# Optimization experiments

Measured on AMD Instinct MI355X. Metric: run time of the kernel, lower is better.

Reference implementation:

```python
import jax, jax.numpy as jnp
import numpy as np

B, T, EMB, HID, NCLS = 256, 512, 128, 256, 32000


def _forward(X, C_table, U_i, V_i, b_i, U_f, V_f, b_f, U_c, V_c, b_c, U_o, V_o, b_o,
             U_i1, V_i1, b_i1, U_f1, V_f1, b_f1, U_c1, V_c1, b_c1, U_o1, V_o1, b_o1,
             W_w, b_out):
    E = C_table[X]  # [B, T, EMB]
    # Layer 0: in the source, h_t0 and c_t0 are NEVER reassigned inside the loop,
    # so they remain zeros for every timestep. Hence h_t0 @ V_* == 0 and
    # f_t * c_t0 == 0, and layer 0 is time-independent -> vectorize over T.
    i0 = jax.nn.sigmoid(jnp.einsum('bte,eh->bth', E, U_i) + b_i)
    g0 = jnp.tanh(jnp.einsum('bte,eh->bth', E, U_c) + b_c)
    o0 = jax.nn.sigmoid(jnp.einsum('bte,eh->bth', E, U_o) + b_o)
    c0 = i0 * g0               # f_t * c_t0 term is exactly zero
    h0 = o0 * jnp.tanh(c0)     # [B, T, HID]

    # Layer 1: true recurrence over its own (h_t1, c_t1) state, fed by layer-0 h.
    # Computed for faithfulness; the source's output ignores it (results holds h_t).
    def step(carry, x):
        h1, c1 = carry
        i1 = jax.nn.sigmoid(x @ U_i1 + h1 @ V_i1 + b_i1)
        g1 = jnp.tanh(x @ U_c1 + h1 @ V_c1 + b_c1)
        f1 = jax.nn.sigmoid(x @ U_f1 + h1 @ V_f1 + b_f1)
        o1 = jax.nn.sigmoid(x @ U_o1 + h1 @ V_o1 + b_o1)
        c1n = f1 * c1 + i1 * g1
        h1n = o1 * jnp.tanh(c1n)
        return (h1n, c1n), None

    zeros = jnp.zeros((h0.shape[0], HID), dtype=h0.dtype)
    _carry, _ = jax.lax.scan(step, (zeros, zeros), jnp.swapaxes(h0, 0, 1))

    # outputs = results[-1] = layer-0 hidden at the last timestep
    logits = h0[:, -1, :] @ W_w.T + b_out  # [B, NCLS]
    return logits


def setup_inputs() -> dict:
    key = jax.random.key(0)
    ks = jax.random.split(key, 32)

    def p(k, *shape):
        return (jax.random.normal(k, shape, dtype=jnp.float32) * 0.02)

    inp = {
        'X': jax.random.randint(ks[0], (B, T), 0, NCLS, dtype=jnp.int32),
        'C_table': p(ks[1], NCLS, EMB),
        'U_i': p(ks[2], EMB, HID), 'V_i': p(ks[3], HID, HID), 'b_i': p(ks[4], HID),
        'U_f': p(ks[5], EMB, HID), 'V_f': p(ks[6], HID, HID), 'b_f': p(ks[7], HID),
        'U_c': p(ks[8], EMB, HID), 'V_c': p(ks[9], HID, HID), 'b_c': p(ks[10], HID),
        'U_o': p(ks[11], EMB, HID), 'V_o': p(ks[12], HID, HID), 'b_o': p(ks[13], HID),
        'U_i1': p(ks[14], HID, HID), 'V_i1': p(ks[15], HID, HID), 'b_i1': p(ks[16], HID),
        'U_f1': p(ks[17], HID, HID), 'V_f1': p(ks[18], HID, HID), 'b_f1': p(ks[19], HID),
        'U_c1': p(ks[20], HID, HID), 'V_c1': p(ks[21], HID, HID), 'b_c1': p(ks[22], HID),
        'U_o1': p(ks[23], HID, HID), 'V_o1': p(ks[24], HID, HID), 'b_o1': p(ks[25], HID),
        'W_w': p(ks[26], NCLS, HID),
        'b_out': jnp.ones((NCLS,), dtype=jnp.float32),
    }
    return inp


def reference(X, C_table, U_i, V_i, b_i, U_f, V_f, b_f, U_c, V_c, b_c, U_o, V_o, b_o,
              U_i1, V_i1, b_i1, U_f1, V_f1, b_f1, U_c1, V_c1, b_c1, U_o1, V_o1, b_o1,
              W_w, b_out):
    return _forward(X, C_table, U_i, V_i, b_i, U_f, V_f, b_f, U_c, V_c, b_c,
                    U_o, V_o, b_o, U_i1, V_i1, b_i1, U_f1, V_f1, b_f1,
                    U_c1, V_c1, b_c1, U_o1, V_o1, b_o1, W_w, b_out)
```

## Files before the change

kernel.cpp:

```cpp
#include <hip/hip_runtime.h>

#define B_SZ   256
#define T_SZ   512
#define EMB    128
#define HID    256
#define NCLS   32000

typedef __attribute__((ext_vector_type(8))) short short8;
typedef __attribute__((ext_vector_type(4))) float f32x4;

__device__ inline unsigned short bf16rne(float f) {
    union { float f; unsigned int u; } v; v.f = f;
    unsigned int u = v.u;
    u += 0x7FFFu + ((u >> 16) & 1u);
    return (unsigned short)(u >> 16);
}

__device__ inline unsigned pkhi(float lo, float hi) {
    union { float f; unsigned u; } a, b;
    a.f = lo; b.f = hi;
    return ((b.u + 0x8000u) & 0xFFFF0000u) | ((a.u + 0x8000u) >> 16);
}

__global__ __launch_bounds__(256)
void lstm_h_last(const int* __restrict__ X, const float* __restrict__ C_table,
                 const float* __restrict__ U_i, const float* __restrict__ b_i,
                 const float* __restrict__ U_c, const float* __restrict__ b_c,
                 const float* __restrict__ U_o, const float* __restrict__ b_o,
                 unsigned short* __restrict__ hws) {
    __shared__ float e[EMB];
    const int m = blockIdx.x;
    const int k = threadIdx.x;

    const int token = X[(size_t)m * T_SZ + (T_SZ - 1)];
    if (k < EMB) e[k] = C_table[(size_t)token * EMB + k];
    __syncthreads();

    float ai = 0.f, ac = 0.f, ao = 0.f;
    #pragma unroll
    for (int c = 0; c < 4; ++c) {
        float ui[32], uc[32], uo[32];
        #pragma unroll
        for (int j = 0; j < 32; ++j) {
            const int ee = c * 32 + j;
            ui[j] = U_i[ee * HID + k];
            uc[j] = U_c[ee * HID + k];
            uo[j] = U_o[ee * HID + k];
        }
        #pragma unroll
        for (int j = 0; j < 32; ++j)
            asm volatile("" : "+v"(ui[j]), "+v"(uc[j]), "+v"(uo[j]));
        #pragma unroll
        for (int j = 0; j < 32; ++j) {
            const float ev = e[c * 32 + j];
            ai += ev * ui[j]; ac += ev * uc[j]; ao += ev * uo[j];
        }
    }

    const float i0 = 1.f / (1.f + expf(-(ai + b_i[k])));
    const float g0 = tanhf(ac + b_c[k]);
    const float o0 = 1.f / (1.f + expf(-(ao + b_o[k])));
    hws[(size_t)m * HID + k] = bf16rne(o0 * tanhf(i0 * g0));
}

#define BN2 64
#define BK  32

__global__ __launch_bounds__(512, 4)
void logits_gemm(const unsigned short* __restrict__ hws,
                 const float* __restrict__ Ww,
                 const float* __restrict__ b_out,
                 float* __restrict__ out) {
    __shared__ float          Wb[3][BN2 * BK];
    __shared__ unsigned short Hb[3][B_SZ * BK];

    const int t    = threadIdx.x;
    const int wid  = t >> 6;
    const int lane = t & 63;
    const int l15  = lane & 15;
    const int lq   = lane >> 4;

    const int n0 = blockIdx.x * BN2;
    const int m0 = wid * 32;

    auto stageW = [&](int ks, float* wb) {
        const unsigned gu = (lane & 7) ^ (lane >> 3);
        const float* src = Ww + (size_t)(n0 + (wid << 3) + (lane >> 3)) * HID
                              + ks * BK + gu * 4;
        __builtin_amdgcn_global_load_lds(
            (const __attribute__((address_space(1))) unsigned int*)src,
            (__attribute__((address_space(3))) unsigned int*)(wb + (wid << 3) * BK),
            16, 0, 0);
    };
    auto stageH = [&](int ks, unsigned short* hb) {
        #pragma unroll
        for (int ii = 0; ii < 2; ++ii) {
            const int i = (wid << 1) + ii;
            const unsigned gu = (lane & 3) ^ ((lane >> 2) & 3);
            const unsigned short* src = hws + (size_t)((i << 4) + (lane >> 2)) * HID
                                            + ks * BK + gu * 8;
            __builtin_amdgcn_global_load_lds(
                (const __attribute__((address_space(1))) unsigned int*)src,
                (__attribute__((address_space(3))) unsigned int*)(hb + (i << 4) * BK),
                16, 0, 0);
        }
    };

    f32x4 acc[2][4] = {};

    auto computeK = [&](const float* wb, const unsigned short* hb) {
        short8 bh[2];
        #pragma unroll
        for (int mf = 0; mf < 2; ++mf) {
            const int r = m0 + (mf << 4) + l15;
            bh[mf] = *reinterpret_cast<const short8*>(
                hb + r * BK + ((lq ^ (r & 3)) << 3));
        }
        #pragma unroll
        for (int nt = 0; nt < 4; ++nt) {
            const int r  = (nt << 4) + l15;
            const int sw = r & 7;
            const float* rp = wb + r * BK;
            f32x4 w0 = *reinterpret_cast<const f32x4*>(rp + ((((lq << 1)    ) ^ sw) << 2));
            f32x4 w1 = *reinterpret_cast<const f32x4*>(rp + ((((lq << 1) | 1) ^ sw) << 2));
            union { short8 s; unsigned u[4]; } p;
            p.u[0] = pkhi(w0[0], w0[1]);
            p.u[1] = pkhi(w0[2], w0[3]);
            p.u[2] = pkhi(w1[0], w1[1]);
            p.u[3] = pkhi(w1[2], w1[3]);
            #pragma unroll
            for (int mf = 0; mf < 2; ++mf)
                acc[mf][nt] = __builtin_amdgcn_mfma_f32_16x16x32_bf16(
                    p.s, bh[mf], acc[mf][nt], 0, 0, 0);
        }
    };

    stageW(0, Wb[0]); stageH(0, Hb[0]);
    stageW(1, Wb[1]); stageH(1, Hb[1]);

#define KITER(ks, N) do {                                          \
    asm volatile("s_waitcnt vmcnt(" #N ")" ::: "memory");          \
    __builtin_amdgcn_s_barrier();                                  \
    __builtin_amdgcn_sched_barrier(0);                             \
    if ((ks) + 2 < 8) {                                            \
        stageW((ks) + 2, Wb[((ks) + 2) % 3]);                      \
        stageH((ks) + 2, Hb[((ks) + 2) % 3]);                      \
    }                                                              \
    computeK(Wb[(ks) % 3], Hb[(ks) % 3]);                          \
} while (0)

    KITER(0, 3); KITER(1, 3); KITER(2, 3); KITER(3, 3);
    KITER(4, 3); KITER(5, 3); KITER(6, 3); KITER(7, 0);
#undef KITER

    #pragma unroll
    for (int nt = 0; nt < 4; ++nt) {
        const int nc = n0 + (nt << 4) + (lq << 2);
        f32x4 bv = *reinterpret_cast<const f32x4*>(b_out + nc);
        #pragma unroll
        for (int mf = 0; mf < 2; ++mf) {
            f32x4 o = acc[mf][nt] + bv;
            *reinterpret_cast<f32x4*>(
                out + (size_t)(m0 + (mf << 4) + l15) * NCLS + nc) = o;
        }
    }
}

extern "C" void kernel_launch(void* const* d_in, const int* in_sizes, int n_in,
                              void* d_out, int out_size, void* d_ws, size_t ws_size,
                              hipStream_t stream) {
    const int*   X       = (const int*)  d_in[0];
    const float* C_table = (const float*)d_in[1];
    const float* U_i     = (const float*)d_in[2];
    const float* b_i     = (const float*)d_in[4];
    const float* U_c     = (const float*)d_in[8];
    const float* b_c     = (const float*)d_in[10];
    const float* U_o     = (const float*)d_in[11];
    const float* b_o     = (const float*)d_in[13];
    const float* W_w     = (const float*)d_in[26];
    const float* b_out   = (const float*)d_in[27];
    float* out = (float*)d_out;

    unsigned short* hws = (unsigned short*)d_ws;

    lstm_h_last<<<B_SZ, 256, 0, stream>>>(X, C_table, U_i, b_i, U_c, b_c,
                                          U_o, b_o, hws);
    logits_gemm<<<NCLS / BN2, 512, 0, stream>>>(hws, W_w, b_out, out);
}
```

Baseline: 30.39 us.

## Stage full H in LDS in MFMA fragment layout, keep W in registers

The first kernel now writes h in a pre-swizzled MFMA-fragment order, so the GEMM can copy all of H (128KB bf16) into LDS with contiguous loads. Each wave loads its 16 W rows over the full K directly into registers and converts them to bf16 once. It then loops over all 256 M rows, which removes the 3-stage K pipeline and the per-iteration barriers. Each block covers 128 columns instead of 64. The cost is 128KB of LDS per block, which limits occupancy, and a large register footprint.

```diff
diff --git a/kernel.cpp b/kernel.cpp
--- a/kernel.cpp
+++ b/kernel.cpp
@@ -21,6 +21,7 @@
     a.f = lo; b.f = hi;
     return ((b.u + 0x8000u) & 0xFFFF0000u) | ((a.u + 0x8000u) >> 16);
 }
+
 
 __global__ __launch_bounds__(256)
 void lstm_h_last(const int* __restrict__ X, const float* __restrict__ C_table,
@@ -60,19 +61,19 @@
     const float i0 = 1.f / (1.f + expf(-(ai + b_i[k])));
     const float g0 = tanhf(ac + b_c[k]);
     const float o0 = 1.f / (1.f + expf(-(ao + b_o[k])));
-    hws[(size_t)m * HID + k] = bf16rne(o0 * tanhf(i0 * g0));
+    const unsigned short hv = bf16rne(o0 * tanhf(i0 * g0));
+
+    const int frag_id = (m >> 4) * 8 + (k >> 5);
+    const int lane_in = ((k >> 3) & 3) * 16 + (m & 15);
+    hws[frag_id * 512 + lane_in * 8 + (k & 7)] = hv;
 }
 
-#define BN2 64
-#define BK  32
-
-__global__ __launch_bounds__(512, 4)
+__global__ __launch_bounds__(512, 2)
 void logits_gemm(const unsigned short* __restrict__ hws,
                  const float* __restrict__ Ww,
                  const float* __restrict__ b_out,
                  float* __restrict__ out) {
-    __shared__ float          Wb[3][BN2 * BK];
-    __shared__ unsigned short Hb[3][B_SZ * BK];
+    __shared__ unsigned short Hs[B_SZ * HID];
 
     const int t    = threadIdx.x;
     const int wid  = t >> 6;
@@ -80,89 +81,62 @@
     const int l15  = lane & 15;
     const int lq   = lane >> 4;
 
-    const int n0 = blockIdx.x * BN2;
-    const int m0 = wid * 32;
+    const int nbase = blockIdx.x * 128 + wid * 16;
 
-    auto stageW = [&](int ks, float* wb) {
-        const unsigned gu = (lane & 7) ^ (lane >> 3);
-        const float* src = Ww + (size_t)(n0 + (wid << 3) + (lane >> 3)) * HID
-                              + ks * BK + gu * 4;
-        __builtin_amdgcn_global_load_lds(
-            (const __attribute__((address_space(1))) unsigned int*)src,
-            (__attribute__((address_space(3))) unsigned int*)(wb + (wid << 3) * BK),
-            16, 0, 0);
-    };
-    auto stageH = [&](int ks, unsigned short* hb) {
-        #pragma unroll
-        for (int ii = 0; ii < 2; ++ii) {
-            const int i = (wid << 1) + ii;
-            const unsigned gu = (lane & 3) ^ ((lane >> 2) & 3);
-            const unsigned short* src = hws + (size_t)((i << 4) + (lane >> 2)) * HID
-                                            + ks * BK + gu * 8;
-            __builtin_amdgcn_global_load_lds(
-                (const __attribute__((address_space(1))) unsigned int*)src,
-                (__attribute__((address_space(3))) unsigned int*)(hb + (i << 4) * BK),
-                16, 0, 0);
-        }
-    };
-
-    f32x4 acc[2][4] = {};
-
-    auto computeK = [&](const float* wb, const unsigned short* hb) {
-        short8 bh[2];
-        #pragma unroll
-        for (int mf = 0; mf < 2; ++mf) {
-            const int r = m0 + (mf << 4) + l15;
-            bh[mf] = *reinterpret_cast<const short8*>(
-                hb + r * BK + ((lq ^ (r & 3)) << 3));
-        }
-        #pragma unroll
-        for (int nt = 0; nt < 4; ++nt) {
-            const int r  = (nt << 4) + l15;
-            const int sw = r & 7;
-            const float* rp = wb + r * BK;
-            f32x4 w0 = *reinterpret_cast<const f32x4*>(rp + ((((lq << 1)    ) ^ sw) << 2));
-            f32x4 w1 = *reinterpret_cast<const f32x4*>(rp + ((((lq << 1) | 1) ^ sw) << 2));
-            union { short8 s; unsigned u[4]; } p;
-            p.u[0] = pkhi(w0[0], w0[1]);
-            p.u[1] = pkhi(w0[2], w0[3]);
-            p.u[2] = pkhi(w1[0], w1[1]);
-            p.u[3] = pkhi(w1[2], w1[3]);
-            #pragma unroll
-            for (int mf = 0; mf < 2; ++mf)
-                acc[mf][nt] = __builtin_amdgcn_mfma_f32_16x16x32_bf16(
-                    p.s, bh[mf], acc[mf][nt], 0, 0, 0);
-        }
-    };
-
-    stageW(0, Wb[0]); stageH(0, Hb[0]);
-    stageW(1, Wb[1]); stageH(1, Hb[1]);
-
-#define KITER(ks, N) do {                                          \
-    asm volatile("s_waitcnt vmcnt(" #N ")" ::: "memory");          \
-    __builtin_amdgcn_s_barrier();                                  \
-    __builtin_amdgcn_sched_barrier(0);                             \
-    if ((ks) + 2 < 8) {                                            \
-        stageW((ks) + 2, Wb[((ks) + 2) % 3]);                      \
-        stageH((ks) + 2, Hb[((ks) + 2) % 3]);                      \
-    }                                                              \
-    computeK(Wb[(ks) % 3], Hb[(ks) % 3]);                          \
-} while (0)
-
-    KITER(0, 3); KITER(1, 3); KITER(2, 3); KITER(3, 3);
-    KITER(4, 3); KITER(5, 3); KITER(6, 3); KITER(7, 0);
-#undef KITER
+    const float* wrow = Ww + (size_t)(nbase + l15) * HID + lq * 8;
+    f32x4 wf[16];
+    #pragma unroll
+    for (int ks = 0; ks < 8; ++ks) {
+        wf[2 * ks]     = *reinterpret_cast<const f32x4*>(wrow + ks * 32);
+        wf[2 * ks + 1] = *reinterpret_cast<const f32x4*>(wrow + ks * 32 + 4);
+    }
 
     #pragma unroll
-    for (int nt = 0; nt < 4; ++nt) {
-        const int nc = n0 + (nt << 4) + (lq << 2);
-        f32x4 bv = *reinterpret_cast<const f32x4*>(b_out + nc);
+    for (int j = 0; j < 16; ++j) {
+        const unsigned short* src = hws + (wid * 16 + j) * 512;
+        __builtin_amdgcn_global_load_lds(
+            (const __attribute__((address_space(1))) unsigned int*)(src + lane * 8),
+            (__attribute__((address_space(3))) unsigned int*)(Hs + (wid * 16 + j) * 512),
+            16, 0, 0);
+    }
+
+    #pragma unroll
+    for (int i = 0; i < 16; ++i) asm volatile("" : "+v"(wf[i]));
+    asm volatile("s_waitcnt vmcnt(0)" ::: "memory");
+    __builtin_amdgcn_s_barrier();
+    __builtin_amdgcn_sched_barrier(0);
+
+    short8 aw[8];
+    #pragma unroll
+    for (int ks = 0; ks < 8; ++ks) {
+        union { short8 s; unsigned u[4]; } p;
+        p.u[0] = pkhi(wf[2 * ks][0],     wf[2 * ks][1]);
+        p.u[1] = pkhi(wf[2 * ks][2],     wf[2 * ks][3]);
+        p.u[2] = pkhi(wf[2 * ks + 1][0], wf[2 * ks + 1][1]);
+        p.u[3] = pkhi(wf[2 * ks + 1][2], wf[2 * ks + 1][3]);
+        aw[ks] = p.s;
+    }
+
+    f32x4 bv = *reinterpret_cast<const f32x4*>(b_out + nbase + lq * 4);
+
+    const unsigned short* hbase = Hs + lane * 8;
+    f32x4 acc[16] = {};
+    #pragma unroll
+    for (int ks = 0; ks < 8; ++ks) {
         #pragma unroll
-        for (int mf = 0; mf < 2; ++mf) {
-            f32x4 o = acc[mf][nt] + bv;
-            *reinterpret_cast<f32x4*>(
-                out + (size_t)(m0 + (mf << 4) + l15) * NCLS + nc) = o;
+        for (int mf = 0; mf < 16; ++mf) {
+            short8 bh = *reinterpret_cast<const short8*>(
+                hbase + (mf * 8 + ks) * 512);
+            acc[mf] = __builtin_amdgcn_mfma_f32_16x16x32_bf16(
+                aw[ks], bh, acc[mf], 0, 0, 0);
         }
+    }
+
+    #pragma unroll
+    for (int mf = 0; mf < 16; ++mf) {
+        f32x4 o = acc[mf] + bv;
+        *reinterpret_cast<f32x4*>(
+            out + (size_t)(mf * 16 + l15) * NCLS + nbase + lq * 4) = o;
     }
 }
 
@@ -185,5 +159,5 @@
 
     lstm_h_last<<<B_SZ, 256, 0, stream>>>(X, C_table, U_i, b_i, U_c, b_c,
                                           U_o, b_o, hws);
-    logits_gemm<<<NCLS / BN2, 512, 0, stream>>>(hws, W_w, b_out, out);
+    logits_gemm<<<NCLS / 128, 512, 0, stream>>>(hws, W_w, b_out, out);
 }
```

Result: no change. 30.14 us (-0.8%).
